# Kernel tuning notes

Measured on AMD Instinct MI355X. Metric: run time of the kernel, lower is better.

Reference implementation:

```python
import jax, jax.numpy as jnp
import numpy as np

B, S, E, H = 2, 2048, 1024, 16
D = E // H  # head_dim = 64


def setup_inputs() -> dict:
    key = jax.random.key(0)
    k1, k2, k3 = jax.random.split(key, 3)
    scale_in = 1.0 / np.sqrt(E)
    return {
        "x": jax.random.normal(k1, (B, S, E), dtype=jnp.float32),
        "W_attn": jax.random.normal(k2, (E, 3 * E), dtype=jnp.float32) * scale_in,
        "b_attn": jnp.zeros((3 * E,), dtype=jnp.float32),
        "W_proj": jax.random.normal(k3, (E, E), dtype=jnp.float32) * scale_in,
        "b_proj": jnp.zeros((E,), dtype=jnp.float32),
    }


def reference(x, W_attn, b_attn, W_proj, b_proj):
    # c_attn: fused QKV projection  [B,S,E] -> [B,S,3E]
    qkv = x @ W_attn + b_attn
    q, k, v = jnp.split(qkv, 3, axis=-1)
    # split heads -> [B,S,H,D]
    q = q.reshape(B, S, H, D)
    k = k.reshape(B, S, H, D)
    v = v.reshape(B, S, H, D)
    # scaled dot-product attention (no causal mask in the source module)
    scores = jnp.einsum("bqhd,bkhd->bhqk", q, k) / jnp.sqrt(jnp.float32(D))
    attn = jax.nn.softmax(scores, axis=-1)  # attn_dropout is identity in eval
    y = jnp.einsum("bhqk,bkhd->bqhd", attn, v).reshape(B, S, E)
    # c_proj; resid_dropout is identity in eval
    return y @ W_proj + b_proj
```

## Files before the change

### kernel.cpp

```cpp
#include <hip/hip_runtime.h>
#include <stdint.h>

#define NB 2
#define NS 2048
#define NE 1024
#define NH 16
#define ND 64
#define NE3 3072
#define NBS 4096
#define NT 32

typedef _Float16 half8 __attribute__((ext_vector_type(8)));
typedef __fp16 fp16x2 __attribute__((ext_vector_type(2)));
typedef float f32x4 __attribute__((ext_vector_type(4)));
typedef float f32x16 __attribute__((ext_vector_type(16)));
typedef unsigned int u32;

__device__ __forceinline__ void gload16(const void* g, void* l) {
  __builtin_amdgcn_global_load_lds(
      (__attribute__((address_space(1))) void*)const_cast<void*>(g),
      (__attribute__((address_space(3))) void*)l, 16, 0, 0);
}

__global__ void k_cvt16(const float* __restrict__ src, _Float16* __restrict__ dst, int n8) {
  int i = blockIdx.x * blockDim.x + threadIdx.x;
  if (i >= n8) return;
  const float4* s = (const float4*)src + (size_t)i * 2;
  float4 a = s[0], b = s[1];
  half8 o;
  o[0]=(_Float16)a.x; o[1]=(_Float16)a.y; o[2]=(_Float16)a.z; o[3]=(_Float16)a.w;
  o[4]=(_Float16)b.x; o[5]=(_Float16)b.y; o[6]=(_Float16)b.z; o[7]=(_Float16)b.w;
  *((half8*)dst + i) = o;
}

__global__ void k_cvtT2(const float* __restrict__ srcA, _Float16* __restrict__ dstA,
                        const float* __restrict__ srcB, _Float16* __restrict__ dstB) {
  __shared__ _Float16 tile[64][72];
  int bx = blockIdx.x;
  const float* src; _Float16* dst; int N;
  if (bx < 48) { src = srcA; dst = dstA; N = NE3; }
  else         { src = srcB; dst = dstB; N = NE; bx -= 48; }
  const int K = NE;
  int n0 = bx * 64, k0 = blockIdx.y * 64;
  int t = threadIdx.x;
  int kk = t >> 2, nc = (t & 3) << 4;
  const float* sp = src + (size_t)(k0 + kk) * N + n0 + nc;
#pragma unroll
  for (int j = 0; j < 16; j += 4) {
    float4 v = *(const float4*)(sp + j);
    tile[kk][nc + j + 0] = (_Float16)v.x;
    tile[kk][nc + j + 1] = (_Float16)v.y;
    tile[kk][nc + j + 2] = (_Float16)v.z;
    tile[kk][nc + j + 3] = (_Float16)v.w;
  }
  __syncthreads();
  int nn = t >> 2, kc = (t & 3) << 4;
  half8 o0, o1;
#pragma unroll
  for (int j = 0; j < 8; ++j) { o0[j] = tile[kc + j][nn]; o1[j] = tile[kc + 8 + j][nn]; }
  _Float16* op = dst + (size_t)(n0 + nn) * K + k0 + kc;
  *(half8*)op = o0;
  *(half8*)(op + 8) = o1;
}

template <int OUT_HALF, int BM>
__global__ __launch_bounds__(256, 2)
void k_gemm(const _Float16* __restrict__ A, const _Float16* __restrict__ Bt,
            const float* __restrict__ bias, void* __restrict__ Cv,
            int M, int N, int K) {
  constexpr int ACH = BM / 16;
  constexpr int CHUNKS = ACH + 8;
  constexpr int PER_WAVE = CHUNKS / 4;
  constexpr int JN = (BM == 128) ? 4 : 2;
  __shared__ _Float16 As[2][BM * 32];
  __shared__ _Float16 Bs[2][128 * 32];
  const int nwg = gridDim.x * gridDim.y;
  const int d = blockIdx.y * gridDim.x + blockIdx.x;
  const int lid = (d & 7) * (nwg >> 3) + (d >> 3);
  const int bx = lid % gridDim.x, by = lid / gridDim.x;
  const int m0 = by * BM, n0 = bx * 128;
  const int t = threadIdx.x, l = t & 63, w = t >> 6;
  const int wr = (BM == 128) ? (w >> 1) : 0;
  const int wc = (BM == 128) ? (w & 1) : w;
  const int srow = l >> 2;
  const int sk = (l & 3) << 3;
  f32x4 acc[4][JN] = {};

#define G_STAGE(KT, BUF)                                                              \
  {                                                                                   \
    _Pragma("unroll")                                                                 \
    for (int p = 0; p < PER_WAVE; ++p) {                                              \
      int cid = w * PER_WAVE + p;                                                     \
      if (cid < ACH)                                                                  \
        gload16(A + (size_t)(m0 + cid * 16 + srow) * K + (KT) * 32 + sk,              \
                (char*)&As[BUF][0] + cid * 1024);                                     \
      else                                                                            \
        gload16(Bt + (size_t)(n0 + (cid - ACH) * 16 + srow) * K + (KT) * 32 + sk,     \
                (char*)&Bs[BUF][0] + (cid - ACH) * 1024);                             \
    }                                                                                 \
  }

  const int T = K / 32;
  G_STAGE(0, 0);
  G_STAGE(1, 1);
  for (int tt = 0; tt < T; ++tt) {
    if (tt + 1 < T) {
      if constexpr (PER_WAVE == 4) asm volatile("s_waitcnt vmcnt(4)" ::: "memory");
      else                         asm volatile("s_waitcnt vmcnt(3)" ::: "memory");
    } else {
      asm volatile("s_waitcnt vmcnt(0)" ::: "memory");
    }
    __builtin_amdgcn_s_barrier();
    asm volatile("" ::: "memory");
    const int cur = tt & 1;
    const _Float16* as = &As[cur][0];
    const _Float16* bs = &Bs[cur][0];
    half8 a[4], b[JN];
#pragma unroll
    for (int i = 0; i < 4; ++i)
      a[i] = *(const half8*)(as + (wr * 64 + i * 16 + (l & 15)) * 32 + ((l >> 4) << 3));
#pragma unroll
    for (int j = 0; j < JN; ++j)
      b[j] = *(const half8*)(bs + ((BM == 128 ? wc * 64 : wc * 32) + j * 16 + (l & 15)) * 32 + ((l >> 4) << 3));
#pragma unroll
    for (int i = 0; i < 4; ++i)
#pragma unroll
      for (int j = 0; j < JN; ++j)
        acc[i][j] = __builtin_amdgcn_mfma_f32_16x16x32_f16(a[i], b[j], acc[i][j], 0, 0, 0);
    asm volatile("s_waitcnt lgkmcnt(0)" ::: "memory");
    __builtin_amdgcn_s_barrier();
    asm volatile("" ::: "memory");
    if (tt + 2 < T) G_STAGE(tt + 2, cur);
  }
#undef G_STAGE

  float bv[JN];
#pragma unroll
  for (int j = 0; j < JN; ++j)
    bv[j] = bias[n0 + (BM == 128 ? wc * 64 : wc * 32) + j * 16 + (l & 15)];
#pragma unroll
  for (int i = 0; i < 4; ++i) {
    int row0 = m0 + wr * 64 + i * 16 + ((l >> 4) << 2);
#pragma unroll
    for (int j = 0; j < JN; ++j) {
      int col = n0 + (BM == 128 ? wc * 64 : wc * 32) + j * 16 + (l & 15);
#pragma unroll
      for (int r = 0; r < 4; ++r) {
        float v = acc[i][j][r] + bv[j];
        if (OUT_HALF) {
          if (col < NE) v *= 0.18033688011112042f;
          ((_Float16*)Cv)[(size_t)(row0 + r) * N + col] = (_Float16)v;
        } else {
          ((float*)Cv)[(size_t)(row0 + r) * N + col] = v;
        }
      }
    }
  }
}

__global__ void k_vt(const _Float16* __restrict__ qkv, _Float16* __restrict__ Vt) {
  __shared__ _Float16 tile[64][72];
  int s0 = blockIdx.x * 64;
  int bh = blockIdx.y, b = bh >> 4, h = bh & 15;
  int t = threadIdx.x;
  int ss = t >> 2, dc = (t & 3) << 4;
  const _Float16* sp = qkv + (size_t)(b * NS + s0 + ss) * NE3 + 2 * NE + h * ND + dc;
  half8 v0 = *(const half8*)sp, v1 = *(const half8*)(sp + 8);
#pragma unroll
  for (int j = 0; j < 8; ++j) { tile[ss][dc + j] = v0[j]; tile[ss][dc + 8 + j] = v1[j]; }
  __syncthreads();
  int d = t >> 2, sc = (t & 3) << 4;
  half8 o0, o1;
#pragma unroll
  for (int j = 0; j < 8; ++j) { o0[j] = tile[sc + j][d]; o1[j] = tile[sc + 8 + j][d]; }
  _Float16* op = Vt + (size_t)(bh * ND + d) * NS + s0 + sc;
  *(half8*)op = o0;
  *(half8*)(op + 8) = o1;
}

__global__ __launch_bounds__(256, 2)
void k_attn(const _Float16* __restrict__ qkv, const _Float16* __restrict__ Vt,
            _Float16* __restrict__ Y) {
  __shared__ _Float16 Kb[2][64 * 64];
  __shared__ _Float16 Vb[2][64 * 64];
  const int dly = blockIdx.y * gridDim.x + blockIdx.x;
  const int lid = (dly & 7) * 64 + (dly >> 3);
  const int bh = lid >> 4, qb = lid & 15;
  const int q0 = qb * 128;
  const int b = bh >> 4, h = bh & 15;
  const int t = threadIdx.x, l = t & 63, w = t >> 6;
  const int c = l & 31, hh = l >> 5;

  half8 qf[4];
  {
    const _Float16* qp = qkv + (size_t)(b * NS + q0 + w * 32 + c) * NE3 + h * ND + 8 * hh;
    qf[0] = *(const half8*)(qp);
    qf[1] = *(const half8*)(qp + 16);
    qf[2] = *(const half8*)(qp + 32);
    qf[3] = *(const half8*)(qp + 48);
  }

  f32x16 Oa0 = {}, Oa1 = {}, Osum = {};
  f32x16 saE0, saE1, saO0, saO1;
  half8 ones;
#pragma unroll
  for (int j = 0; j < 8; ++j) ones[j] = (_Float16)1.0f;

  const int lh4 = l >> 4;
  const int ls7 = (l >> 1) & 7;
  const int l1 = l & 1;
  const int grp = c >> 1;
  const int xr = grp & 7;

#define RD_BASE (grp * 256 + ((c & 1) << 4))

#define STAGE_K(KT, BUF)                                                             \
  {                                                                                  \
    _Pragma("unroll")                                                                \
    for (int i = 0; i < 2; ++i) {                                                    \
      int ci = w * 2 + i;                                                            \
      int g = 4 * ci + lh4;                                                          \
      int row = 2 * g + l1;                                                          \
      int j8 = (ls7 ^ (g & 7)) << 3;                                                 \
      gload16(qkv + (size_t)(b * NS + (KT) * 64 + row) * NE3 + NE + h * ND + j8,     \
              (char*)&Kb[BUF][0] + ci * 1024);                                       \
    }                                                                                \
  }
#define STAGE_V(KT, BUF)                                                             \
  {                                                                                  \
    _Pragma("unroll")                                                                \
    for (int i = 0; i < 2; ++i) {                                                    \
      int ci = w * 2 + i;                                                            \
      int g = 4 * ci + lh4;                                                          \
      int row = 2 * g + l1;                                                          \
      int j8 = (ls7 ^ (g & 7)) << 3;                                                 \
      gload16(Vt + (size_t)(bh * ND + row) * NS + (KT) * 64 + j8,                    \
              (char*)&Vb[BUF][0] + ci * 1024);                                       \
    }                                                                                \
  }

#define QK_TILE(BUF, SA0, SA1)                                                       \
  {                                                                                  \
    SA0 = (f32x16){}; SA1 = (f32x16){};                                              \
    _Pragma("unroll")                                                                \
    for (int tt = 0; tt < 4; ++tt) {                                                 \
      int off = RD_BASE + (((2 * tt + hh) ^ xr) << 5);                               \
      half8 kf0 = *(const half8*)((char*)&Kb[BUF][0] + off);                         \
      half8 kf1 = *(const half8*)((char*)&Kb[BUF][0] + off + 4096);                  \
      SA0 = __builtin_amdgcn_mfma_f32_32x32x16_f16(kf0, qf[tt], SA0, 0, 0, 0);       \
      SA1 = __builtin_amdgcn_mfma_f32_32x32x16_f16(kf1, qf[tt], SA1, 0, 0, 0);       \
    }                                                                                \
  }

#define PVSTEP(KK, DARR, CUR)                                                         \
    {                                                                                 \
      u32 pb0 = DARR[2 * ((KK) & 1)][0], pa0 = DARR[2 * ((KK) & 1) + 1][0];           \
      u32 pb1 = DARR[2 * ((KK) & 1)][1], pa1 = DARR[2 * ((KK) & 1) + 1][1];           \
      u32 sent0 = hh ? pb0 : pa0;                                                     \
      u32 sent1 = hh ? pb1 : pa1;                                                     \
      u32 recv0 = __shfl_xor(sent0, 32);                                              \
      u32 recv1 = __shfl_xor(sent1, 32);                                              \
      union { u32 d[4]; half8 h; } pfu;                                               \
      pfu.d[0] = hh ? recv0 : pb0;                                                    \
      pfu.d[1] = hh ? recv1 : pb1;                                                    \
      pfu.d[2] = hh ? pa0 : recv0;                                                    \
      pfu.d[3] = hh ? pa1 : recv1;                                                    \
      int offv = RD_BASE + (((2 * (KK) + hh) ^ xr) << 5);                             \
      half8 vf0 = *(const half8*)((char*)&Vb[CUR][0] + offv);                         \
      half8 vf1 = *(const half8*)((char*)&Vb[CUR][0] + offv + 4096);                  \
      Oa0 = __builtin_amdgcn_mfma_f32_32x32x16_f16(pfu.h, vf0, Oa0, 0, 0, 0);         \
      Oa1 = __builtin_amdgcn_mfma_f32_32x32x16_f16(pfu.h, vf1, Oa1, 0, 0, 0);         \
      Osum = __builtin_amdgcn_mfma_f32_32x32x16_f16(pfu.h, ones, Osum, 0, 0, 0);      \
    }

#define TILE_BODY(T, CUR, SAC0, SAC1, SAN0, SAN1)                                     \
  {                                                                                   \
    u32 D0[4][2], D1[4][2];                                                           \
    _Pragma("unroll")                                                                 \
    for (int s = 0; s < 4; ++s) {                                                     \
      fp16x2 e0 = __builtin_amdgcn_cvt_pkrtz(__builtin_amdgcn_exp2f(SAC0[4 * s + 0]), \
                                             __builtin_amdgcn_exp2f(SAC0[4 * s + 1]));\
      fp16x2 e1 = __builtin_amdgcn_cvt_pkrtz(__builtin_amdgcn_exp2f(SAC0[4 * s + 2]), \
                                             __builtin_amdgcn_exp2f(SAC0[4 * s + 3]));\
      fp16x2 e2 = __builtin_amdgcn_cvt_pkrtz(__builtin_amdgcn_exp2f(SAC1[4 * s + 0]), \
                                             __builtin_amdgcn_exp2f(SAC1[4 * s + 1]));\
      fp16x2 e3 = __builtin_amdgcn_cvt_pkrtz(__builtin_amdgcn_exp2f(SAC1[4 * s + 2]), \
                                             __builtin_amdgcn_exp2f(SAC1[4 * s + 3]));\
      D0[s][0] = __builtin_bit_cast(u32, e0);                                         \
      D0[s][1] = __builtin_bit_cast(u32, e1);                                         \
      D1[s][0] = __builtin_bit_cast(u32, e2);                                         \
      D1[s][1] = __builtin_bit_cast(u32, e3);                                         \
    }                                                                                 \
    if ((T) + 1 < NT) QK_TILE((CUR) ^ 1, SAN0, SAN1);                                 \
    PVSTEP(0, D0, CUR)                                                                \
    PVSTEP(1, D0, CUR)                                                                \
    PVSTEP(2, D1, CUR)                                                                \
    PVSTEP(3, D1, CUR)                                                                \
    __syncthreads();                                                                  \
    if ((T) + 2 < NT) STAGE_V((T) + 2, CUR);                                          \
    if ((T) + 3 < NT) STAGE_K((T) + 3, (CUR) ^ 1);                                    \
  }

  STAGE_K(0, 0);
  STAGE_V(0, 0);
  STAGE_K(1, 1);
  __syncthreads();
  QK_TILE(0, saE0, saE1);
  __syncthreads();
  STAGE_V(1, 1);
  STAGE_K(2, 0);

  for (int kt = 0; kt < NT; kt += 2) {
    TILE_BODY(kt, 0, saE0, saE1, saO0, saO1);
    TILE_BODY(kt + 1, 1, saO0, saO1, saE0, saE1);
  }
#undef TILE_BODY
#undef PVSTEP
#undef QK_TILE
#undef STAGE_K
#undef STAGE_V
#undef RD_BASE

#pragma unroll
  for (int i = 0; i < 16; ++i) {
    int ql = (i & 3) + 8 * (i >> 2) + 4 * hh;
    float inv = 1.0f / Osum[i];
    size_t base = (size_t)(b * NS + q0 + w * 32 + ql) * NE + h * ND + c;
    Y[base] = (_Float16)(Oa0[i] * inv);
    Y[base + 32] = (_Float16)(Oa1[i] * inv);
  }
}

extern "C" void kernel_launch(void* const* d_in, const int* in_sizes, int n_in,
                              void* d_out, int out_size, void* d_ws, size_t ws_size,
                              hipStream_t stream) {
  (void)in_sizes; (void)n_in; (void)out_size; (void)ws_size;
  const float* x      = (const float*)d_in[0];
  const float* W_attn = (const float*)d_in[1];
  const float* b_attn = (const float*)d_in[2];
  const float* W_proj = (const float*)d_in[3];
  const float* b_proj = (const float*)d_in[4];
  char* ws = (char*)d_ws;
  const size_t MB = 1024 * 1024;
  _Float16* qkvb = (_Float16*)(ws);
  _Float16* WaT  = (_Float16*)(ws + 24 * MB);
  _Float16* WpT  = (_Float16*)(ws + 30 * MB);
  _Float16* xb   = (_Float16*)(ws + 32 * MB);
  _Float16* Vt   = (_Float16*)(ws + 40 * MB);
  _Float16* yb   = (_Float16*)(ws + 32 * MB);

  k_cvt16<<<dim3(2048), dim3(256), 0, stream>>>(x, xb, NBS * NE / 8);
  k_cvtT2<<<dim3(64, 16), dim3(256), 0, stream>>>(W_attn, WaT, W_proj, WpT);
  k_gemm<1, 128><<<dim3(NE3 / 128, NBS / 128), dim3(256), 0, stream>>>(xb, WaT, b_attn, (void*)qkvb, NBS, NE3, NE);
  k_vt<<<dim3(NS / 64, NB * NH), dim3(256), 0, stream>>>(qkvb, Vt);
  k_attn<<<dim3(NS / 128, NB * NH), dim3(256), 0, stream>>>(qkvb, Vt, yb);
  k_gemm<0, 64><<<dim3(NE / 128, NBS / 64), dim3(256), 0, stream>>>(yb, WpT, b_proj, d_out, NBS, NE, NE);
}
```

Measured before the change: 126.0 us.

## Split attention KV range in two and combine partials in a separate kernel

The attention kernel now splits each query block's key/value range into two halves and launches twice as many blocks. Each block writes unnormalised fp16 partial outputs and per-row exp-sums, using the output buffer and the freed weight workspace as scratch. A new combine kernel adds the two partials and divides by the summed normalisers. The aim is more parallelism and better CU occupancy, with launch bounds raised to 4 blocks per CU. The cost is extra global traffic for the partials, one more kernel launch, and a tighter register budget that may cause spills.

```diff
diff --git a/kernel.cpp b/kernel.cpp
--- a/kernel.cpp
+++ b/kernel.cpp
@@ -8,7 +8,7 @@
 #define ND 64
 #define NE3 3072
 #define NBS 4096
-#define NT 32
+#define NTL 16
 
 typedef _Float16 half8 __attribute__((ext_vector_type(8)));
 typedef __fp16 fp16x2 __attribute__((ext_vector_type(2)));
@@ -178,15 +178,16 @@
   *(half8*)(op + 8) = o1;
 }
 
-__global__ __launch_bounds__(256, 2)
+__global__ __launch_bounds__(256, 4)
 void k_attn(const _Float16* __restrict__ qkv, const _Float16* __restrict__ Vt,
-            _Float16* __restrict__ Y) {
+            _Float16* __restrict__ PO, float* __restrict__ sums) {
   __shared__ _Float16 Kb[2][64 * 64];
   __shared__ _Float16 Vb[2][64 * 64];
   const int dly = blockIdx.y * gridDim.x + blockIdx.x;
-  const int lid = (dly & 7) * 64 + (dly >> 3);
-  const int bh = lid >> 4, qb = lid & 15;
+  const int lid = (dly & 7) * 128 + (dly >> 3);
+  const int bh = lid >> 5, qb = (lid >> 1) & 15, sp = lid & 1;
   const int q0 = qb * 128;
+  const int kbase = sp * NTL;
   const int b = bh >> 4, h = bh & 15;
   const int t = threadIdx.x, l = t & 63, w = t >> 6;
   const int c = l & 31, hh = l >> 5;
@@ -214,29 +215,29 @@
 
 #define RD_BASE (grp * 256 + ((c & 1) << 4))
 
-#define STAGE_K(KT, BUF)                                                             \
-  {                                                                                  \
-    _Pragma("unroll")                                                                \
-    for (int i = 0; i < 2; ++i) {                                                    \
-      int ci = w * 2 + i;                                                            \
-      int g = 4 * ci + lh4;                                                          \
-      int row = 2 * g + l1;                                                          \
-      int j8 = (ls7 ^ (g & 7)) << 3;                                                 \
-      gload16(qkv + (size_t)(b * NS + (KT) * 64 + row) * NE3 + NE + h * ND + j8,     \
-              (char*)&Kb[BUF][0] + ci * 1024);                                       \
-    }                                                                                \
-  }
-#define STAGE_V(KT, BUF)                                                             \
-  {                                                                                  \
-    _Pragma("unroll")                                                                \
-    for (int i = 0; i < 2; ++i) {                                                    \
-      int ci = w * 2 + i;                                                            \
-      int g = 4 * ci + lh4;                                                          \
-      int row = 2 * g + l1;                                                          \
-      int j8 = (ls7 ^ (g & 7)) << 3;                                                 \
-      gload16(Vt + (size_t)(bh * ND + row) * NS + (KT) * 64 + j8,                    \
-              (char*)&Vb[BUF][0] + ci * 1024);                                       \
-    }                                                                                \
+#define STAGE_K(KT, BUF)                                                                  \
+  {                                                                                       \
+    _Pragma("unroll")                                                                     \
+    for (int i = 0; i < 2; ++i) {                                                         \
+      int ci = w * 2 + i;                                                                 \
+      int g = 4 * ci + lh4;                                                               \
+      int row = 2 * g + l1;                                                               \
+      int j8 = (ls7 ^ (g & 7)) << 3;                                                      \
+      gload16(qkv + (size_t)(b * NS + (kbase + (KT)) * 64 + row) * NE3 + NE + h * ND + j8,\
+              (char*)&Kb[BUF][0] + ci * 1024);                                            \
+    }                                                                                     \
+  }
+#define STAGE_V(KT, BUF)                                                                  \
+  {                                                                                       \
+    _Pragma("unroll")                                                                     \
+    for (int i = 0; i < 2; ++i) {                                                         \
+      int ci = w * 2 + i;                                                                 \
+      int g = 4 * ci + lh4;                                                               \
+      int row = 2 * g + l1;                                                               \
+      int j8 = (ls7 ^ (g & 7)) << 3;                                                      \
+      gload16(Vt + (size_t)(bh * ND + row) * NS + (kbase + (KT)) * 64 + j8,               \
+              (char*)&Vb[BUF][0] + ci * 1024);                                            \
+    }                                                                                     \
   }
 
 #define QK_TILE(BUF, SA0, SA1)                                                       \
@@ -291,14 +292,14 @@
       D1[s][0] = __builtin_bit_cast(u32, e2);                                         \
       D1[s][1] = __builtin_bit_cast(u32, e3);                                         \
     }                                                                                 \
-    if ((T) + 1 < NT) QK_TILE((CUR) ^ 1, SAN0, SAN1);                                 \
+    if ((T) + 1 < NTL) QK_TILE((CUR) ^ 1, SAN0, SAN1);                                \
     PVSTEP(0, D0, CUR)                                                                \
     PVSTEP(1, D0, CUR)                                                                \
     PVSTEP(2, D1, CUR)                                                                \
     PVSTEP(3, D1, CUR)                                                                \
     __syncthreads();                                                                  \
-    if ((T) + 2 < NT) STAGE_V((T) + 2, CUR);                                          \
-    if ((T) + 3 < NT) STAGE_K((T) + 3, (CUR) ^ 1);                                    \
+    if ((T) + 2 < NTL) STAGE_V((T) + 2, CUR);                                         \
+    if ((T) + 3 < NTL) STAGE_K((T) + 3, (CUR) ^ 1);                                   \
   }
 
   STAGE_K(0, 0);
@@ -310,7 +311,7 @@
   STAGE_V(1, 1);
   STAGE_K(2, 0);
 
-  for (int kt = 0; kt < NT; kt += 2) {
+  for (int kt = 0; kt < NTL; kt += 2) {
     TILE_BODY(kt, 0, saE0, saE1, saO0, saO1);
     TILE_BODY(kt + 1, 1, saO0, saO1, saE0, saE1);
   }
@@ -324,11 +325,31 @@
 #pragma unroll
   for (int i = 0; i < 16; ++i) {
     int ql = (i & 3) + 8 * (i >> 2) + 4 * hh;
-    float inv = 1.0f / Osum[i];
-    size_t base = (size_t)(b * NS + q0 + w * 32 + ql) * NE + h * ND + c;
-    Y[base] = (_Float16)(Oa0[i] * inv);
-    Y[base + 32] = (_Float16)(Oa1[i] * inv);
-  }
+    int qg = q0 + w * 32 + ql;
+    size_t base = (size_t)(sp * NBS + b * NS + qg) * NE + h * ND + c;
+    PO[base] = (_Float16)Oa0[i];
+    PO[base + 32] = (_Float16)Oa1[i];
+    if (c == 0) sums[(sp * 32 + bh) * NS + qg] = Osum[i];
+  }
+}
+
+__global__ void k_combine(const _Float16* __restrict__ PO, const float* __restrict__ sums,
+                          _Float16* __restrict__ yb) {
+  int idx = blockIdx.x * blockDim.x + threadIdx.x;
+  if (idx >= NBS * NE / 8) return;
+  int row = idx >> 7;
+  int e = (idx & 127) << 3;
+  int h = e >> 6;
+  int b = row >> 11;
+  int q = row & (NS - 1);
+  int bh = b * NH + h;
+  float inv = 1.0f / (sums[bh * NS + q] + sums[(32 + bh) * NS + q]);
+  half8 o0 = *((const half8*)PO + idx);
+  half8 o1 = *((const half8*)(PO + (size_t)NBS * NE) + idx);
+  half8 y;
+#pragma unroll
+  for (int j = 0; j < 8; ++j) y[j] = (_Float16)(((float)o0[j] + (float)o1[j]) * inv);
+  *((half8*)yb + idx) = y;
 }
 
 extern "C" void kernel_launch(void* const* d_in, const int* in_sizes, int n_in,
@@ -344,15 +365,18 @@
   const size_t MB = 1024 * 1024;
   _Float16* qkvb = (_Float16*)(ws);
   _Float16* WaT  = (_Float16*)(ws + 24 * MB);
+  float*    sums = (float*)(ws + 24 * MB);
   _Float16* WpT  = (_Float16*)(ws + 30 * MB);
   _Float16* xb   = (_Float16*)(ws + 32 * MB);
   _Float16* Vt   = (_Float16*)(ws + 40 * MB);
   _Float16* yb   = (_Float16*)(ws + 32 * MB);
+  _Float16* PO   = (_Float16*)d_out;
 
   k_cvt16<<<dim3(2048), dim3(256), 0, stream>>>(x, xb, NBS * NE / 8);
   k_cvtT2<<<dim3(64, 16), dim3(256), 0, stream>>>(W_attn, WaT, W_proj, WpT);
   k_gemm<1, 128><<<dim3(NE3 / 128, NBS / 128), dim3(256), 0, stream>>>(xb, WaT, b_attn, (void*)qkvb, NBS, NE3, NE);
   k_vt<<<dim3(NS / 64, NB * NH), dim3(256), 0, stream>>>(qkvb, Vt);
-  k_attn<<<dim3(NS / 128, NB * NH), dim3(256), 0, stream>>>(qkvb, Vt, yb);
+  k_attn<<<dim3(2 * NS / 128, NB * NH), dim3(256), 0, stream>>>(qkvb, Vt, PO, sums);
+  k_combine<<<dim3(NBS * NE / 8 / 256), dim3(256), 0, stream>>>(PO, sums, yb);
   k_gemm<0, 64><<<dim3(NE / 128, NBS / 64), dim3(256), 0, stream>>>(yb, WpT, b_proj, d_out, NBS, NE, NE);
 }
```

Result: slower. 189.5 us (+50.4%).
